# Kernel tuning notes

Measured on AMD Instinct MI355X. Metric: run time of the kernel, lower is better.

Reference implementation:

```python
import jax, jax.numpy as jnp
import numpy as np
import math

B, H, S, DK = 4, 16, 2048, 64

def setup_inputs() -> dict:
    key = jax.random.key(0)
    kq, kk, kv, km = jax.random.split(key, 4)
    q = jax.random.normal(kq, (B, H, S, DK), dtype=jnp.float32)
    k = jax.random.normal(kk, (B, H, S, DK), dtype=jnp.float32)
    v = jax.random.normal(kv, (B, H, S, DK), dtype=jnp.float32)
    mask = jax.random.randint(km, (B, 1, 1, S), 0, 2, dtype=jnp.int32)
    return {"q": q, "k": k, "v": v, "mask": mask}

def reference(q, k, v, mask):
    scale = 1.0 / math.sqrt(DK)
    # scores: [B, H, S, S]
    scores = jnp.einsum('bhqd,bhkd->bhqk', q, k) * scale
    scores = jnp.where(mask == 0, jnp.float32(-1e9), scores)
    attn = jax.nn.softmax(scores, axis=-1)
    out = jnp.einsum('bhqk,bhkd->bhqd', attn, v)
    return out
```

## Files before the change

### kernel.cpp

```cpp
#include <hip/hip_runtime.h>
#include <hip/hip_bf16.h>

#define S_LEN 2048
#define D_K   64
#define N_H   16
#define N_B   4
#define KVB   64
#define QPB   256
#define NQB   (S_LEN / QPB)
#define NBH   (N_B * N_H)
#define WS_NEED (2L * NBH * S_LEN * D_K * 2 + 4L * S_LEN * 4 + 16)

typedef __attribute__((ext_vector_type(8)))  short bf16x8;
typedef __attribute__((ext_vector_type(16))) float f32x16;
typedef unsigned int u32;
typedef __attribute__((ext_vector_type(4))) u32 u32x4;

__device__ inline short f2bfs(float x) {
    __hip_bfloat16 h = __float2bfloat16(x);
    return __builtin_bit_cast(short, h);
}

__device__ inline bf16x8 cvt8(const float* __restrict__ p) {
    float4 a = *(const float4*)p;
    float4 b = *(const float4*)(p + 4);
    bf16x8 f;
    f[0] = f2bfs(a.x); f[1] = f2bfs(a.y);
    f[2] = f2bfs(a.z); f[3] = f2bfs(a.w);
    f[4] = f2bfs(b.x); f[5] = f2bfs(b.y);
    f[6] = f2bfs(b.z); f[7] = f2bfs(b.w);
    return f;
}

__device__ inline bf16x8 cvt8s(const float* __restrict__ p, float s) {
    float4 a = *(const float4*)p;
    float4 b = *(const float4*)(p + 4);
    bf16x8 f;
    f[0] = f2bfs(a.x * s); f[1] = f2bfs(a.y * s);
    f[2] = f2bfs(a.z * s); f[3] = f2bfs(a.w * s);
    f[4] = f2bfs(b.x * s); f[5] = f2bfs(b.y * s);
    f[6] = f2bfs(b.z * s); f[7] = f2bfs(b.w * s);
    return f;
}

__device__ inline int vswz(int d) { return ((d & 7) ^ ((d >> 3) & 7)) << 4; }

__device__ inline void gld16(const void* g, void* l) {
    __builtin_amdgcn_global_load_lds(
        (const __attribute__((address_space(1))) void*)g,
        (__attribute__((address_space(3))) void*)l, 16, 0, 0);
}

__global__ __launch_bounds__(64)
void mask_scan(const int* __restrict__ mask, int* __restrict__ idx,
               int* __restrict__ cnt) {
    const int b = blockIdx.x, lane = threadIdx.x;
    const int* mb = mask + b * S_LEN;
    int base = 0;
    for (int j0 = 0; j0 < S_LEN; j0 += 64) {
        int mv = mb[j0 + lane];
        unsigned long long ball = __ballot(mv != 0);
        int pos = base + __popcll(ball & ((1ull << lane) - 1ull));
        if (mv) idx[b * S_LEN + pos] = j0 + lane;
        base += __popcll(ball);
    }
    if (lane == 0) cnt[b] = base;
}

__global__ __launch_bounds__(256)
void gather_cvt(const float* __restrict__ k, const float* __restrict__ v,
                const int* __restrict__ idx, const int* __restrict__ cnt,
                short* __restrict__ kc, short* __restrict__ vt) {
    const int bid = blockIdx.x, bh = bid >> 5, i0 = (bid & 31) * 64;
    const int b = bh >> 4;
    const int m = cnt[b];
    if (i0 >= ((m + 63) & ~63)) return;
    const int t = threadIdx.x;
    const int r = t >> 2, c0 = (t & 3) * 16;
    const int i = i0 + r;

    __shared__ __align__(16) short tile_[64][72];
    bf16x8 fv0, fv1, fk0, fk1;
    if (i < m) {
        const int src = idx[b * S_LEN + i];
        const float* kp = k + ((long)bh * S_LEN + src) * D_K + c0;
        const float* vp = v + ((long)bh * S_LEN + src) * D_K + c0;
        fk0 = cvt8(kp); fk1 = cvt8(kp + 8);
        fv0 = cvt8(vp); fv1 = cvt8(vp + 8);
    } else {
#pragma unroll
        for (int j = 0; j < 8; ++j) { fk0[j] = 0; fk1[j] = 0; fv0[j] = 0; fv1[j] = 0; }
    }
    short* kdst = kc + ((long)bh * S_LEN + i) * D_K + c0;
    *(bf16x8*)kdst       = fk0;
    *(bf16x8*)(kdst + 8) = fk1;
    *(bf16x8*)&tile_[r][c0]     = fv0;
    *(bf16x8*)&tile_[r][c0 + 8] = fv1;
    __syncthreads();
    const int dd = t >> 2, k0 = (t & 3) * 16;
    bf16x8 h0, h1;
#pragma unroll
    for (int j = 0; j < 8; ++j) {
        h0[j] = tile_[k0 + j][dd];
        h1[j] = tile_[k0 + 8 + j][dd];
    }
    short* dst = vt + ((long)bh * D_K + dd) * S_LEN + i0 + k0;
    *(bf16x8*)dst       = h0;
    *(bf16x8*)(dst + 8) = h1;
}

__global__ __launch_bounds__(512)
void attn_fwd(const float* __restrict__ q, const short* __restrict__ kbf,
              const short* __restrict__ vtb, const int* __restrict__ cnt,
              float* __restrict__ out) {
    const int id      = blockIdx.x;
    const int logical = (id & 7) * 64 + (id >> 3);
    const int bh      = logical >> 3;
    const int qblk    = logical & 7;
    const int b       = bh >> 4;
    const int t       = threadIdx.x;
    const int lane    = t & 63;
    const int wq      = t >> 6;
    const int hb      = lane >> 5;
    const int ql      = lane & 31;

    const int m   = cnt[b];
    const int NTr = (m + 63) >> 6;

    __shared__ __align__(16) short kbuf[2][KVB * D_K];
    __shared__ __align__(16) short vbuf[2][D_K * KVB];

    const float scale2 = 0.125f * 1.44269504f;
    const long  baseq  = (long)bh * S_LEN * D_K;
    const int   qrow0  = qblk * QPB + wq * 32;

    bf16x8 qf[4];
    {
        const float* qp = q + baseq + (long)(qrow0 + ql) * D_K + hb * 8;
#pragma unroll
        for (int kd = 0; kd < 4; ++kd) qf[kd] = cvt8s(qp + kd * 16, scale2);
    }

    const int lrow = lane >> 3, lchk = lane & 7;
    const int rA = wq * 8 + lrow;
    const short* ksA = kbf + baseq + (long)rA * D_K + ((lchk ^ (rA & 7)) * 8);
    const short* vsA = vtb + ((long)bh * D_K + rA) * S_LEN
                       + ((lchk ^ ((rA & 7) ^ ((rA >> 3) & 7))) * 8);

    auto STAGE_K = [&](int sel) {
        gld16(ksA, (char*)&kbuf[sel][0] + (wq * 8) * 128);
        ksA += KVB * D_K;
    };
    auto STAGE_V = [&](int sel) {
        gld16(vsA, (char*)&vbuf[sel][0] + (wq * 8) * 128);
        vsA += KVB;
    };

    f32x16 o0, o1;
#pragma unroll
    for (int r = 0; r < 16; ++r) { o0[r] = 0.f; o1[r] = 0.f; }
    float lrun = 0.f;

    f32x16 st0, st1;

    auto QK = [&](int kv0, int sel, bool lastt) {
        const char* kbp = (const char*)&kbuf[sel][0];
        f32x16 a0, a1;
        if (!lastt) {
#pragma unroll
            for (int r = 0; r < 16; ++r) { a0[r] = 0.f; a1[r] = 0.f; }
        } else {
            int keyb = kv0 + 4 * hb;
#pragma unroll
            for (int r = 0; r < 16; ++r) {
                int key = keyb + (r & 3) + 8 * (r >> 2);
                a0[r] = (key < m)      ? 0.f : -1e9f;
                a1[r] = (key + 32 < m) ? 0.f : -1e9f;
            }
        }
        int rb0 = (ql) * 128,      sz0 = (ql & 7) << 4;
        int rb1 = (32 + ql) * 128, sz1 = sz0;
        __builtin_amdgcn_s_setprio(1);
#pragma unroll
        for (int kd = 0; kd < 4; ++kd) {
            int co = (kd * 16 + hb * 8) * 2;
            bf16x8 kf0 = *(const bf16x8*)(kbp + ((rb0 + co) ^ sz0));
            bf16x8 kf1 = *(const bf16x8*)(kbp + ((rb1 + co) ^ sz1));
            a0 = __builtin_amdgcn_mfma_f32_32x32x16_bf16(kf0, qf[kd], a0, 0, 0, 0);
            a1 = __builtin_amdgcn_mfma_f32_32x32x16_bf16(kf1, qf[kd], a1, 0, 0, 0);
        }
        __builtin_amdgcn_s_setprio(0);
        st0 = a0; st1 = a1;
    };

    STAGE_K(0);
    STAGE_V(0);
    if (NTr > 1) STAGE_K(1);
    __syncthreads();
    QK(0, 0, NTr == 1);
    __syncthreads();

    for (int tt = 0; tt < NTr; ++tt) {
        if (tt + 2 < NTr) STAGE_K(tt & 1);
        if (tt + 1 < NTr) STAGE_V((tt + 1) & 1);

        u32 w[2][8];
        float rs0 = 0.f, rs1 = 0.f;
#pragma unroll
        for (int mm = 0; mm < 8; ++mm) {
            float p0 = __builtin_amdgcn_exp2f(st0[2 * mm]);
            float p1 = __builtin_amdgcn_exp2f(st0[2 * mm + 1]);
            rs0 += p0; rs1 += p1;
            u32 r;
            asm("v_cvt_pk_bf16_f32 %0, %1, %2" : "=v"(r) : "v"(p0), "v"(p1));
            w[0][mm] = r;
        }
#pragma unroll
        for (int mm = 0; mm < 8; ++mm) {
            float p0 = __builtin_amdgcn_exp2f(st1[2 * mm]);
            float p1 = __builtin_amdgcn_exp2f(st1[2 * mm + 1]);
            rs0 += p0; rs1 += p1;
            u32 r;
            asm("v_cvt_pk_bf16_f32 %0, %1, %2" : "=v"(r) : "v"(p0), "v"(p1));
            w[1][mm] = r;
        }
        float rs = rs0 + rs1;
        rs += __shfl_xor(rs, 32, 64);
        lrun += rs;

        if (tt + 1 < NTr) QK((tt + 1) * KVB, (tt + 1) & 1, tt + 2 == NTr);

        const char* vbp = (const char*)&vbuf[tt & 1][0];
#pragma unroll
        for (int kbi = 0; kbi < 4; ++kbi) {
            int c = kbi >> 1, a2 = (kbi & 1) * 4;
            u32 x0 = w[c][a2 + 0], y0 = w[c][a2 + 2];
            u32 x1 = w[c][a2 + 1], y1 = w[c][a2 + 3];
            asm("v_permlane32_swap_b32 %0, %1" : "+v"(x0), "+v"(y0));
            asm("v_permlane32_swap_b32 %0, %1" : "+v"(x1), "+v"(y1));
            u32x4 av = {x0, x1, y0, y1};
            bf16x8 pa = __builtin_bit_cast(bf16x8, av);
            __builtin_amdgcn_s_setprio(1);
#pragma unroll
            for (int dn = 0; dn < 2; ++dn) {
                int d = dn * 32 + ql;
                bf16x8 vf = *(const bf16x8*)(vbp +
                              ((d * 128 + (kbi * 16 + hb * 8) * 2) ^ vswz(d)));
                if (dn == 0)
                    o0 = __builtin_amdgcn_mfma_f32_32x32x16_bf16(pa, vf, o0, 0, 0, 0);
                else
                    o1 = __builtin_amdgcn_mfma_f32_32x32x16_bf16(pa, vf, o1, 0, 0, 0);
            }
            __builtin_amdgcn_s_setprio(0);
        }

        __syncthreads();
    }

    float rl = 1.0f / lrun;
#pragma unroll
    for (int r = 0; r < 16; ++r) {
        int   cr  = (r & 3) + 8 * (r >> 2) + 4 * hb;
        float rlr = __shfl(rl, cr, 64);
        long  rowb = baseq + (long)(qrow0 + cr) * D_K;
        out[rowb + ql]      = o0[r] * rlr;
        out[rowb + 32 + ql] = o1[r] * rlr;
    }
}

__global__ __launch_bounds__(256)
void attn_fwd_legacy(const float* __restrict__ q, const float* __restrict__ k,
                     const float* __restrict__ v, const int* __restrict__ mask,
                     float* __restrict__ out) {
    const int id      = blockIdx.x;
    const int logical = (id & 7) * 128 + (id >> 3);
    const int bh      = logical >> 4;
    const int qblk    = logical & 15;
    const int b       = bh >> 4;
    const int t       = threadIdx.x;
    const int lane    = t & 63;
    const int wq      = t >> 6;
    const int hb      = lane >> 5;
    const int ql      = lane & 31;

    __shared__ __align__(16) short kbuf[KVB * D_K];
    __shared__ __align__(16) short vtbuf[D_K * KVB];
    __shared__ float mbias[S_LEN];

    const float scale2 = 0.125f * 1.44269504f;
    const long  base   = (long)bh * S_LEN * D_K;
    const int   qrow0  = qblk * 128 + wq * 32;

    {
        const int* mb = mask + b * S_LEN;
        for (int i = t; i < S_LEN; i += 256)
            mbias[i] = mb[i] ? 0.f : -1.442695e9f;
    }

    bf16x8 qf[4];
    {
        const float* qp = q + base + (long)(qrow0 + ql) * D_K + hb * 8;
#pragma unroll
        for (int kd = 0; kd < 4; ++kd) qf[kd] = cvt8s(qp + kd * 16, 1.0f);
    }

    f32x16 o0, o1;
#pragma unroll
    for (int r = 0; r < 16; ++r) { o0[r] = 0.f; o1[r] = 0.f; }
    float mrun = -1e30f, lrun = 0.f;

    const int srow = t >> 3;
    const int scol = t & 7;
    float4 kr[2][2], vr[2][2];

    auto LOADT = [&](int kv0) {
#pragma unroll
        for (int u2 = 0; u2 < 2; ++u2) {
            int row = srow + u2 * 32;
            const float* kp = k + base + (long)(kv0 + row) * D_K + scol * 8;
            const float* vp = v + base + (long)(kv0 + row) * D_K + scol * 8;
            kr[u2][0] = *(const float4*)kp; kr[u2][1] = *(const float4*)(kp + 4);
            vr[u2][0] = *(const float4*)vp; vr[u2][1] = *(const float4*)(vp + 4);
        }
    };

    LOADT(0);

    for (int tt = 0; tt < S_LEN / KVB; ++tt) {
        const int kv0 = tt * KVB;
        __syncthreads();
#pragma unroll
        for (int u2 = 0; u2 < 2; ++u2) {
            int row = srow + u2 * 32;
            bf16x8 fk, fv;
#pragma unroll
            for (int j = 0; j < 4; ++j) {
                fk[j]     = f2bfs(((const float*)&kr[u2][0])[j]);
                fk[j + 4] = f2bfs(((const float*)&kr[u2][1])[j]);
                fv[j]     = f2bfs(((const float*)&vr[u2][0])[j]);
                fv[j + 4] = f2bfs(((const float*)&vr[u2][1])[j]);
            }
            int kbyte = (row * 128 + scol * 16) ^ ((row & 7) << 4);
            *(bf16x8*)((char*)kbuf + kbyte) = fk;
#pragma unroll
            for (int j = 0; j < 8; ++j) {
                int d = scol * 8 + j;
                *(short*)((char*)vtbuf + ((d * 128 + row * 2) ^ vswz(d))) = fv[j];
            }
        }
        if (tt + 1 < S_LEN / KVB) LOADT(kv0 + KVB);
        __syncthreads();

        f32x16 stl[2];
#pragma unroll
        for (int kb32 = 0; kb32 < 2; ++kb32) {
            f32x16 acc;
#pragma unroll
            for (int r = 0; r < 16; ++r) acc[r] = 0.f;
            int krow = kb32 * 32 + ql;
            int rb = krow * 128, sz = (krow & 7) << 4;
#pragma unroll
            for (int kd = 0; kd < 4; ++kd) {
                bf16x8 kf = *(const bf16x8*)((const char*)kbuf + ((rb + (kd * 16 + hb * 8) * 2) ^ sz));
                acc = __builtin_amdgcn_mfma_f32_32x32x16_bf16(kf, qf[kd], acc, 0, 0, 0);
            }
            stl[kb32] = acc;
        }
#pragma unroll
        for (int kb32 = 0; kb32 < 2; ++kb32)
#pragma unroll
            for (int r = 0; r < 16; ++r) {
                int key = kv0 + kb32 * 32 + (r & 3) + 8 * (r >> 2) + 4 * hb;
                stl[kb32][r] = fmaf(stl[kb32][r], scale2, mbias[key]);
            }

        float m8[8];
#pragma unroll
        for (int i = 0; i < 8; ++i)
            m8[i] = fmaxf(fmaxf(stl[0][i], stl[0][i + 8]),
                          fmaxf(stl[1][i], stl[1][i + 8]));
        float tmax = fmaxf(fmaxf(fmaxf(m8[0], m8[1]), fmaxf(m8[2], m8[3])),
                           fmaxf(fmaxf(m8[4], m8[5]), fmaxf(m8[6], m8[7])));
        tmax = fmaxf(tmax, __shfl_xor(tmax, 32, 64));

        if (__any(tmax > mrun + 10.0f)) {
            float mnew = fmaxf(mrun, tmax);
            float al   = __builtin_amdgcn_exp2f(mrun - mnew);
            mrun = mnew;
            lrun *= al;
#pragma unroll
            for (int r = 0; r < 16; ++r) {
                float ar = __shfl(al, (r & 3) + 8 * (r >> 2) + 4 * hb, 64);
                o0[r] *= ar; o1[r] *= ar;
            }
        }

        u32 w[2][8];
        float rs = 0.f;
#pragma unroll
        for (int kb32 = 0; kb32 < 2; ++kb32)
#pragma unroll
            for (int mm = 0; mm < 8; ++mm) {
                float p0 = __builtin_amdgcn_exp2f(stl[kb32][2 * mm]     - mrun);
                float p1 = __builtin_amdgcn_exp2f(stl[kb32][2 * mm + 1] - mrun);
                rs += p0 + p1;
                w[kb32][mm] = (u32)(unsigned short)f2bfs(p0) |
                              ((u32)(unsigned short)f2bfs(p1) << 16);
            }
        rs += __shfl_xor(rs, 32, 64);
        lrun += rs;

#pragma unroll
        for (int kbi = 0; kbi < 4; ++kbi) {
            int c = kbi >> 1, a2 = (kbi & 1) * 4;
            u32 x0 = w[c][a2 + 0], y0 = w[c][a2 + 2];
            u32 x1 = w[c][a2 + 1], y1 = w[c][a2 + 3];
            asm("v_permlane32_swap_b32 %0, %1" : "+v"(x0), "+v"(y0));
            asm("v_permlane32_swap_b32 %0, %1" : "+v"(x1), "+v"(y1));
            u32x4 av = {x0, x1, y0, y1};
            bf16x8 pa = __builtin_bit_cast(bf16x8, av);
#pragma unroll
            for (int dn = 0; dn < 2; ++dn) {
                int d = dn * 32 + ql;
                bf16x8 vf = *(const bf16x8*)((const char*)vtbuf +
                              ((d * 128 + (kbi * 16 + hb * 8) * 2) ^ vswz(d)));
                if (dn == 0)
                    o0 = __builtin_amdgcn_mfma_f32_32x32x16_bf16(pa, vf, o0, 0, 0, 0);
                else
                    o1 = __builtin_amdgcn_mfma_f32_32x32x16_bf16(pa, vf, o1, 0, 0, 0);
            }
        }
    }

    float rl = 1.0f / lrun;
#pragma unroll
    for (int r = 0; r < 16; ++r) {
        int   cr  = (r & 3) + 8 * (r >> 2) + 4 * hb;
        float rlr = __shfl(rl, cr, 64);
        long  rowb = base + (long)(qrow0 + cr) * D_K;
        out[rowb + ql]      = o0[r] * rlr;
        out[rowb + 32 + ql] = o1[r] * rlr;
    }
}

extern "C" void kernel_launch(void* const* d_in, const int* in_sizes, int n_in,
                              void* d_out, int out_size, void* d_ws, size_t ws_size,
                              hipStream_t stream) {
    const float* q    = (const float*)d_in[0];
    const float* k    = (const float*)d_in[1];
    const float* v    = (const float*)d_in[2];
    const int*   mask = (const int*)d_in[3];
    float*       out  = (float*)d_out;

    if (ws_size >= (size_t)WS_NEED) {
        short* kc  = (short*)d_ws;
        short* vt  = kc + (long)NBH * S_LEN * D_K;
        int*   idx = (int*)(vt + (long)NBH * S_LEN * D_K);
        int*   cnt = idx + 4 * S_LEN;
        mask_scan<<<dim3(N_B), 64, 0, stream>>>(mask, idx, cnt);
        gather_cvt<<<dim3(NBH * (S_LEN / 64)), 256, 0, stream>>>(k, v, idx, cnt, kc, vt);
        attn_fwd<<<dim3(NQB * NBH), 512, 0, stream>>>(q, kc, vt, cnt, out);
    } else {
        attn_fwd_legacy<<<dim3((S_LEN / 128) * NBH), 256, 0, stream>>>(q, k, v, mask, out);
    }
}
```

Before: 83.12 us.

## Deepen K/V LDS ring buffers and process two KV tiles per barrier

New measurement: 80.80 us. 1.03x faster.

```diff
diff --git a/kernel.cpp b/kernel.cpp
--- a/kernel.cpp
+++ b/kernel.cpp
@@ -127,8 +127,8 @@
     const int m   = cnt[b];
     const int NTr = (m + 63) >> 6;
 
-    __shared__ __align__(16) short kbuf[2][KVB * D_K];
-    __shared__ __align__(16) short vbuf[2][D_K * KVB];
+    __shared__ __align__(16) short kbuf[5][KVB * D_K];
+    __shared__ __align__(16) short vbuf[4][D_K * KVB];
 
     const float scale2 = 0.125f * 1.44269504f;
     const long  baseq  = (long)bh * S_LEN * D_K;
@@ -147,13 +147,13 @@
     const short* vsA = vtb + ((long)bh * D_K + rA) * S_LEN
                        + ((lchk ^ ((rA & 7) ^ ((rA >> 3) & 7))) * 8);
 
-    auto STAGE_K = [&](int sel) {
-        gld16(ksA, (char*)&kbuf[sel][0] + (wq * 8) * 128);
-        ksA += KVB * D_K;
-    };
-    auto STAGE_V = [&](int sel) {
-        gld16(vsA, (char*)&vbuf[sel][0] + (wq * 8) * 128);
-        vsA += KVB;
+    auto STAGE_K = [&](int i) {
+        gld16(ksA + (long)i * (KVB * D_K),
+              (char*)kbuf + (i % 5) * (KVB * D_K * 2) + (wq * 8) * 128);
+    };
+    auto STAGE_V = [&](int i) {
+        gld16(vsA + (long)i * KVB,
+              (char*)vbuf + (i % 4) * (D_K * KVB * 2) + (wq * 8) * 128);
     };
 
     f32x16 o0, o1;
@@ -161,31 +161,43 @@
     for (int r = 0; r < 16; ++r) { o0[r] = 0.f; o1[r] = 0.f; }
     float lrun = 0.f;
 
+    f32x16 ZEROV;
+#pragma unroll
+    for (int r = 0; r < 16; ++r) ZEROV[r] = 0.f;
+
     f32x16 st0, st1;
 
     auto QK = [&](int kv0, int sel, bool lastt) {
-        const char* kbp = (const char*)&kbuf[sel][0];
+        const char* kbp = (const char*)kbuf + sel * (KVB * D_K * 2);
+        int rb0 = (ql) * 128,      sz0 = (ql & 7) << 4;
+        int rb1 = (32 + ql) * 128;
         f32x16 a0, a1;
-        if (!lastt) {
-#pragma unroll
-            for (int r = 0; r < 16; ++r) { a0[r] = 0.f; a1[r] = 0.f; }
-        } else {
-            int keyb = kv0 + 4 * hb;
-#pragma unroll
-            for (int r = 0; r < 16; ++r) {
-                int key = keyb + (r & 3) + 8 * (r >> 2);
-                a0[r] = (key < m)      ? 0.f : -1e9f;
-                a1[r] = (key + 32 < m) ? 0.f : -1e9f;
-            }
-        }
-        int rb0 = (ql) * 128,      sz0 = (ql & 7) << 4;
-        int rb1 = (32 + ql) * 128, sz1 = sz0;
         __builtin_amdgcn_s_setprio(1);
-#pragma unroll
-        for (int kd = 0; kd < 4; ++kd) {
+        {
+            int co = (hb * 8) * 2;
+            bf16x8 kf0 = *(const bf16x8*)(kbp + ((rb0 + co) ^ sz0));
+            bf16x8 kf1 = *(const bf16x8*)(kbp + ((rb1 + co) ^ sz0));
+            if (!lastt) {
+                a0 = __builtin_amdgcn_mfma_f32_32x32x16_bf16(kf0, qf[0], ZEROV, 0, 0, 0);
+                a1 = __builtin_amdgcn_mfma_f32_32x32x16_bf16(kf1, qf[0], ZEROV, 0, 0, 0);
+            } else {
+                f32x16 c0, c1;
+                int keyb = kv0 + 4 * hb;
+#pragma unroll
+                for (int r = 0; r < 16; ++r) {
+                    int key = keyb + (r & 3) + 8 * (r >> 2);
+                    c0[r] = (key < m)      ? 0.f : -1e9f;
+                    c1[r] = (key + 32 < m) ? 0.f : -1e9f;
+                }
+                a0 = __builtin_amdgcn_mfma_f32_32x32x16_bf16(kf0, qf[0], c0, 0, 0, 0);
+                a1 = __builtin_amdgcn_mfma_f32_32x32x16_bf16(kf1, qf[0], c1, 0, 0, 0);
+            }
+        }
+#pragma unroll
+        for (int kd = 1; kd < 4; ++kd) {
             int co = (kd * 16 + hb * 8) * 2;
             bf16x8 kf0 = *(const bf16x8*)(kbp + ((rb0 + co) ^ sz0));
-            bf16x8 kf1 = *(const bf16x8*)(kbp + ((rb1 + co) ^ sz1));
+            bf16x8 kf1 = *(const bf16x8*)(kbp + ((rb1 + co) ^ sz0));
             a0 = __builtin_amdgcn_mfma_f32_32x32x16_bf16(kf0, qf[kd], a0, 0, 0, 0);
             a1 = __builtin_amdgcn_mfma_f32_32x32x16_bf16(kf1, qf[kd], a1, 0, 0, 0);
         }
@@ -193,18 +205,9 @@
         st0 = a0; st1 = a1;
     };
 
-    STAGE_K(0);
-    STAGE_V(0);
-    if (NTr > 1) STAGE_K(1);
-    __syncthreads();
-    QK(0, 0, NTr == 1);
-    __syncthreads();
-
-    for (int tt = 0; tt < NTr; ++tt) {
-        if (tt + 2 < NTr) STAGE_K(tt & 1);
-        if (tt + 1 < NTr) STAGE_V((tt + 1) & 1);
-
-        u32 w[2][8];
+    u32 w[2][8];
+
+    auto SM = [&]() {
         float rs0 = 0.f, rs1 = 0.f;
 #pragma unroll
         for (int mm = 0; mm < 8; ++mm) {
@@ -227,10 +230,10 @@
         float rs = rs0 + rs1;
         rs += __shfl_xor(rs, 32, 64);
         lrun += rs;
-
-        if (tt + 1 < NTr) QK((tt + 1) * KVB, (tt + 1) & 1, tt + 2 == NTr);
-
-        const char* vbp = (const char*)&vbuf[tt & 1][0];
+    };
+
+    auto PV = [&](int sel) {
+        const char* vbp = (const char*)vbuf + sel * (D_K * KVB * 2);
 #pragma unroll
         for (int kbi = 0; kbi < 4; ++kbi) {
             int c = kbi >> 1, a2 = (kbi & 1) * 4;
@@ -252,6 +255,33 @@
                     o1 = __builtin_amdgcn_mfma_f32_32x32x16_bf16(pa, vf, o1, 0, 0, 0);
             }
             __builtin_amdgcn_s_setprio(0);
+        }
+    };
+
+    STAGE_K(0);
+    STAGE_V(0);
+    if (NTr > 1) { STAGE_K(1); STAGE_V(1); }
+    if (NTr > 2) STAGE_K(2);
+    if (NTr > 3) STAGE_K(3);
+    __syncthreads();
+    QK(0, 0, NTr == 1);
+    __syncthreads();
+
+    for (int u = 0; 2 * u < NTr; ++u) {
+        const int t0 = 2 * u, t1 = 2 * u + 1;
+        if (t0 + 4 < NTr) STAGE_K(t0 + 4);
+        if (t0 + 5 < NTr) STAGE_K(t0 + 5);
+        if (t0 + 2 < NTr) STAGE_V(t0 + 2);
+        if (t0 + 3 < NTr) STAGE_V(t0 + 3);
+
+        SM();
+        if (t0 + 1 < NTr) QK((t0 + 1) * KVB, (t0 + 1) % 5, t0 + 2 == NTr);
+        PV(t0 & 3);
+
+        if (t1 < NTr) {
+            SM();
+            if (t1 + 1 < NTr) QK((t1 + 1) * KVB, (t1 + 1) % 5, t1 + 2 == NTr);
+            PV(t1 & 3);
         }
 
         __syncthreads();
```
